# Kernel optimization log

Hardware: AMD Instinct MI355X
Metric: run time of the kernel (lower is better)

Reference implementation:

```python
import jax, jax.numpy as jnp
import numpy as np

B, S, D_IN, D_MODEL, H = 2, 2048, 1024, 1024, 16
DEPTH = D_MODEL // H


def setup_inputs() -> dict:
    key = jax.random.key(0)
    ks = jax.random.split(key, 12)
    f32 = jnp.float32
    scale = 0.02  # typical init scale for linear weights
    inp = {
        "v": jax.random.normal(ks[0], (B, S, D_IN), f32),
        "k": jax.random.normal(ks[1], (B, S, D_IN), f32),
        "q": jax.random.normal(ks[2], (B, S, D_IN), f32),
        # padding mask: 1 -> masked out, 0 -> keep; broadcastable to (B,H,Sq,Sk)
        "mask": jax.random.randint(ks[3], (B, 1, 1, S), 0, 2).astype(f32),
        # linear params stored as [in, out] so y = x @ W + b (matches torch Linear math)
        "Wq": jax.random.normal(ks[4], (D_IN, D_MODEL), f32) * scale,
        "bq": jnp.zeros((D_MODEL,), f32),
        "Wk": jax.random.normal(ks[5], (D_IN, D_MODEL), f32) * scale,
        "bk": jnp.zeros((D_MODEL,), f32),
        "Wv": jax.random.normal(ks[6], (D_IN, D_MODEL), f32) * scale,
        "bv": jnp.zeros((D_MODEL,), f32),
        "Wo": jax.random.normal(ks[7], (D_MODEL, D_MODEL), f32) * scale,
        "bo": jnp.zeros((D_MODEL,), f32),
    }
    return inp


def _split_heads(x):
    # [B, S, D_MODEL] -> [B, H, S, DEPTH]
    b = x.shape[0]
    return x.reshape(b, -1, H, DEPTH).transpose(0, 2, 1, 3)


def reference(v, k, q, mask, Wq, bq, Wk, bk, Wv, bv, Wo, bo):
    qh = _split_heads(q @ Wq + bq)   # [B,H,Sq,D]
    kh = _split_heads(k @ Wk + bk)   # [B,H,Sk,D]
    vh = _split_heads(v @ Wv + bv)   # [B,H,Sk,D]

    # scaled dot-product attention with additive mask (mask * -1e9)
    inv_sqrt_dk = 1.0 / jnp.sqrt(jnp.float32(DEPTH))
    logits = jnp.einsum('bhqd,bhkd->bhqk', qh, kh) * inv_sqrt_dk
    logits = logits + mask * (-1e9)
    attn = jax.nn.softmax(logits, axis=-1)          # [B,H,Sq,Sk]
    ctx = jnp.einsum('bhqk,bhkd->bhqd', attn, vh)   # [B,H,Sq,D]

    b = q.shape[0]
    concat = ctx.transpose(0, 2, 1, 3).reshape(b, -1, D_MODEL)  # [B,Sq,D_MODEL]
    out = concat @ Wo + bo
    return out, attn
```

## Files before the change

kernel.cpp:

```cpp
#include <hip/hip_runtime.h>
#include <cstdint>
#include <cstddef>

typedef __attribute__((ext_vector_type(4))) float f4;
typedef __attribute__((ext_vector_type(8))) short bf16x8;
typedef __attribute__((ext_vector_type(8))) unsigned short u16x8;
typedef unsigned long long u64;

__device__ __forceinline__ unsigned short f2bf(float x) {
    unsigned u = __float_as_uint(x);
    u += 0x7fffu + ((u >> 16) & 1u);
    return (unsigned short)(u >> 16);
}
__device__ __forceinline__ float bf2f(unsigned short h) {
    return __uint_as_float(((unsigned)h) << 16);
}
__device__ __forceinline__ float fast_exp2(float x) { return __builtin_amdgcn_exp2f(x); }
__device__ __forceinline__ float fast_log2(float x) { return __builtin_amdgcn_logf(x); }
__device__ __forceinline__ void gll16(const void* g, void* l) {
    __builtin_amdgcn_global_load_lds(
        (const __attribute__((address_space(1))) unsigned int*)g,
        (__attribute__((address_space(3))) unsigned int*)l, 16, 0, 0);
}
__device__ __forceinline__ f4 mfma16(bf16x8 a, bf16x8 b, f4 c) {
    return __builtin_amdgcn_mfma_f32_16x16x32_bf16(a, b, c, 0, 0, 0);
}

__global__ __launch_bounds__(256)
void prep_w_kernel(const float* __restrict__ Wq, const float* __restrict__ Wk,
                   const float* __restrict__ Wv, const float* __restrict__ Wo,
                   unsigned short* __restrict__ wt)
{
    const int w = blockIdx.z;
    const float* W = w == 0 ? Wq : (w == 1 ? Wk : (w == 2 ? Wv : Wo));
    unsigned short* hi = wt + (size_t)w * 1048576;

    const int kb = blockIdx.x << 6, nb = blockIdx.y << 6;
    __shared__ float T[64][68];
    const int tid = threadIdx.x;
    {
        const int r = tid >> 2, c0 = (tid & 3) << 4;
        const float* src = W + (size_t)(kb + r) * 1024 + nb + c0;
        *(f4*)&T[r][c0 + 0]  = *(const f4*)(src + 0);
        *(f4*)&T[r][c0 + 4]  = *(const f4*)(src + 4);
        *(f4*)&T[r][c0 + 8]  = *(const f4*)(src + 8);
        *(f4*)&T[r][c0 + 12] = *(const f4*)(src + 12);
    }
    __syncthreads();
    {
        const int n = tid & 63, ks = (tid >> 6) << 4;
        unsigned short vh[16];
        #pragma unroll
        for (int j = 0; j < 16; ++j) vh[j] = f2bf(T[ks + j][n]);
        const size_t dst = (size_t)(nb + n) * 1024 + kb + ks;
        *(u16x8*)(hi + dst)     = *(u16x8*)&vh[0];
        *(u16x8*)(hi + dst + 8) = *(u16x8*)&vh[8];
    }
}

__global__ __launch_bounds__(256)
void prep_a_kernel(const float* __restrict__ q, const float* __restrict__ k,
                   const float* __restrict__ v, unsigned short* __restrict__ a_hi)
{
    const int gid = blockIdx.x * 256 + threadIdx.x;
    const int z = gid >> 18;
    const int rem = gid & 262143;
    const float* src = z == 0 ? q : (z == 1 ? k : v);
    const size_t off = (size_t)rem << 4;
    const float* s = src + off;
    unsigned short* hi = a_hi + ((size_t)z << 22) + off;
    float xs[16];
    *(f4*)&xs[0]  = *(const f4*)(s + 0);
    *(f4*)&xs[4]  = *(const f4*)(s + 4);
    *(f4*)&xs[8]  = *(const f4*)(s + 8);
    *(f4*)&xs[12] = *(const f4*)(s + 12);
    unsigned short hv[16];
    #pragma unroll
    for (int j = 0; j < 16; ++j) hv[j] = f2bf(xs[j]);
    *(u16x8*)(hi + 0) = *(u16x8*)&hv[0];
    *(u16x8*)(hi + 8) = *(u16x8*)&hv[8];
}

__device__ __forceinline__ void gemm1_core(
    const unsigned short* __restrict__ AH, const unsigned short* __restrict__ WH,
    const float* __restrict__ bias, int bm, int bn, int mode,
    unsigned short* __restrict__ o_hi, float* __restrict__ o_f32, unsigned char* lds)
{
    unsigned char* As = lds;
    unsigned char* Bs = lds + 16384;

    const int tid = threadIdx.x, lane = tid & 63, wave = tid >> 6;
    const int wm = wave >> 1, wn = wave & 1;
    const int cx = lane & 15, lg = lane >> 4;
    const int l3 = lane >> 3, p3 = lane & 7;
    const int m0 = bm << 7, n0 = bn << 7;

    f4 acc[4][4];
    #pragma unroll
    for (int i = 0; i < 4; ++i)
        #pragma unroll
        for (int j = 0; j < 4; ++j) acc[i][j] = (f4){0.f, 0.f, 0.f, 0.f};

    #pragma unroll 1
    for (int k0 = 0; k0 < 1024; k0 += 64) {
        __syncthreads();
        #pragma unroll
        for (int c = 0; c < 4; ++c) {
            const int cb = (c << 2) + wave;
            const int row = (cb << 3) + l3;
            const int lgx = p3 ^ (row & 7);
            gll16(AH + (size_t)(m0 + row) * 1024 + k0 + (lgx << 3),
                  As + (cb << 10) + (lane << 4));
            gll16(WH + (size_t)(n0 + row) * 1024 + k0 + (lgx << 3),
                  Bs + (cb << 10) + (lane << 4));
        }
        __syncthreads();
        #pragma unroll
        for (int ks = 0; ks < 2; ++ks) {
            bf16x8 ah[4], bh[4];
            #pragma unroll
            for (int t = 0; t < 4; ++t) {
                const int r = (wm << 6) + (t << 4) + cx;
                ah[t] = *(const bf16x8*)(As + r * 128 + (((((ks << 2) + lg)) ^ (r & 7)) << 4));
                const int n = (wn << 6) + (t << 4) + cx;
                bh[t] = *(const bf16x8*)(Bs + n * 128 + (((((ks << 2) + lg)) ^ (n & 7)) << 4));
            }
            #pragma unroll
            for (int i = 0; i < 4; ++i)
                #pragma unroll
                for (int j = 0; j < 4; ++j)
                    acc[i][j] = mfma16(ah[i], bh[j], acc[i][j]);
        }
    }

    float bv4[4];
    #pragma unroll
    for (int j = 0; j < 4; ++j) bv4[j] = bias[n0 + (wn << 6) + (j << 4) + cx];

    #pragma unroll
    for (int i = 0; i < 4; ++i)
        #pragma unroll
        for (int j = 0; j < 4; ++j) {
            const int n = n0 + (wn << 6) + (j << 4) + cx;
            #pragma unroll
            for (int r = 0; r < 4; ++r) {
                const float val = acc[i][j][r] + bv4[j];
                const int m = m0 + (wm << 6) + (i << 4) + (lg << 2) + r;
                if (mode == 2) {
                    o_f32[(size_t)m * 1024 + n] = val;
                } else {
                    const int b = m >> 11, s = m & 2047, hh = n >> 6, d = n & 63;
                    o_hi[(((size_t)(b * 16 + hh)) * 2048 + s) * 64 + d] = f2bf(val);
                }
            }
        }
}

__global__ __launch_bounds__(256)
void qkv_gemm_kernel(const unsigned short* __restrict__ a_hi,
                     const unsigned short* __restrict__ wt,
                     const float* __restrict__ bq, const float* __restrict__ bk,
                     const float* __restrict__ bv,
                     unsigned short* __restrict__ q_hi, unsigned short* __restrict__ k_hi,
                     unsigned short* __restrict__ v_hi)
{
    __shared__ __align__(16) unsigned char lds[32768];
    const int f = blockIdx.x;
    const int id2 = (f & 7) * 96 + (f >> 3);
    const int z = id2 >> 8;
    const int rem = id2 & 255;
    const int bn = rem >> 5, bm = rem & 31;
    const unsigned short* AH = a_hi + ((size_t)z << 22);
    const unsigned short* WH = wt + (size_t)z * 1048576;
    const float* bias = z == 0 ? bq : (z == 1 ? bk : bv);
    unsigned short* ohi = z == 0 ? q_hi : (z == 1 ? k_hi : v_hi);
    gemm1_core(AH, WH, bias, bm, bn, 1, ohi, nullptr, lds);
}

__global__ __launch_bounds__(256)
void out_gemm_kernel(const unsigned short* __restrict__ ctx_hi,
                     const unsigned short* __restrict__ wt_o,
                     const float* __restrict__ bo, float* __restrict__ out)
{
    __shared__ __align__(16) unsigned char lds[32768];
    const int f = blockIdx.x;
    const int id2 = (f & 7) * 32 + (f >> 3);
    const int bn = id2 >> 5, bm = id2 & 31;
    gemm1_core(ctx_hi, wt_o, bo, bm, bn, 2, nullptr, out, lds);
}

__global__ __launch_bounds__(256, 3)
void attn_kernel(const unsigned short* __restrict__ q_hi, const unsigned short* __restrict__ k_hi,
                 const unsigned short* __restrict__ v_hi, const float* __restrict__ mask,
                 float* __restrict__ attn, unsigned short* __restrict__ ctx_hi)
{
    __shared__ __align__(16) unsigned char lds[49152];
    unsigned char* K1 = lds;
    unsigned char* Vs = lds + 16384;
    unsigned char* Ps = lds + 32768;
    float*         ML = (float*)(lds + 40960);

    const int f = blockIdx.x;
    const int swzf = (f & 7) * 128 + (f >> 3);
    const int bh = swzf >> 5;
    const int q0 = (swzf & 31) << 6;
    const int b = bh >> 4, h = bh & 15;
    const int tid = threadIdx.x, lane = tid & 63, wave = tid >> 6;
    const int cx = lane & 15, lg = lane >> 4;
    const int l3 = lane >> 3, p3 = lane & 7;
    const size_t base = (size_t)bh * 131072;
    const float* mg = mask + (size_t)b * 2048;

    constexpr float C2   = 0.18033688011112042f;
    constexpr float M2   = -1.4426950408889634e9f;
    constexpr float MFIX = 4.0f;

    {
        const int i0 = tid << 3;
        f4 mv0 = *(const f4*)(mg + i0);
        f4 mv1 = *(const f4*)(mg + i0 + 4);
        f4 w0, w1;
        #pragma unroll
        for (int j = 0; j < 4; ++j) { w0[j] = fmaf(mv0[j], M2, -MFIX); w1[j] = fmaf(mv1[j], M2, -MFIX); }
        *(f4*)(ML + i0) = w0;
        *(f4*)(ML + i0 + 4) = w1;
    }
    #pragma unroll
    for (int c = 0; c < 2; ++c) {
        const int cb = (c << 2) + wave;
        const int row = (cb << 3) + l3;
        const int lgx = p3 ^ (row & 7);
        gll16(q_hi + base + (size_t)(q0 + row) * 64 + (lgx << 3),
              Ps + (cb << 10) + (lane << 4));
        gll16(k_hi + base + (size_t)row * 64 + (lgx << 3),
              K1 + (cb << 10) + (lane << 4));
    }
    {
        u16x8 v0 = *(const u16x8*)(v_hi + base + (size_t)lane * 64 + (wave << 4));
        u16x8 v1 = *(const u16x8*)(v_hi + base + (size_t)lane * 64 + (wave << 4) + 8);
        const int slot = lane >> 3, sb = (lane & 7) << 1;
        #pragma unroll
        for (int j = 0; j < 8; ++j) {
            const int d = (wave << 4) + j;
            *(unsigned short*)(Vs + d * 128 + ((slot ^ (d & 7)) << 4) + sb) = (unsigned short)v0[j];
            const int d2 = d + 8;
            *(unsigned short*)(Vs + d2 * 128 + ((slot ^ (d2 & 7)) << 4) + sb) = (unsigned short)v1[j];
        }
    }
    __syncthreads();

    bf16x8 qb[2];
    {
        const int r = (wave << 4) + cx;
        const int mk = r & 7;
        #pragma unroll
        for (int ks = 0; ks < 2; ++ks)
            qb[ks] = *(const bf16x8*)(Ps + r * 128 + (((((ks << 2) + lg)) ^ mk) << 4));
    }

    float l_loc = 0.f;
    #pragma unroll 1
    for (int t = 0; t < 32; ++t) {
        const int p = t & 1;
        const int k0 = t << 6;
        if (t < 31) {
            #pragma unroll
            for (int c = 0; c < 2; ++c) {
                const int cb = (c << 2) + wave;
                const int row = (cb << 3) + l3;
                const int lgx = p3 ^ (row & 7);
                gll16(k_hi + base + (size_t)(k0 + 64 + row) * 64 + (lgx << 3),
                      K1 + ((p ^ 1) << 13) + (cb << 10) + (lane << 4));
            }
        }
        const unsigned char* Kc = K1 + (p << 13);
        #pragma unroll
        for (int nt = 0; nt < 4; ++nt) {
            const int kr = (nt << 4) + cx;
            const int mk = kr & 7;
            f4 s = (f4){0.f, 0.f, 0.f, 0.f};
            #pragma unroll
            for (int ks = 0; ks < 2; ++ks) {
                const bf16x8 kb = *(const bf16x8*)(Kc + kr * 128 + (((((ks << 2) + lg)) ^ mk) << 4));
                s = mfma16(kb, qb[ks], s);
            }
            const f4 mlv = *(const f4*)(ML + k0 + (nt << 4) + (lg << 2));
            l_loc += fast_exp2(fmaf(s[0], C2, mlv[0]))
                   + fast_exp2(fmaf(s[1], C2, mlv[1]))
                   + fast_exp2(fmaf(s[2], C2, mlv[2]))
                   + fast_exp2(fmaf(s[3], C2, mlv[3]));
        }
        asm volatile("s_waitcnt vmcnt(0) lgkmcnt(0)" ::: "memory");
        __builtin_amdgcn_s_barrier();
    }
    float ss = l_loc;
    ss += __shfl_xor(ss, 16);
    ss += __shfl_xor(ss, 32);
    const float ofs2 = fast_log2(ss);

    #pragma unroll
    for (int c = 0; c < 2; ++c) {
        const int cb = (c << 2) + wave;
        const int row = (cb << 3) + l3;
        const int lgx = p3 ^ (row & 7);
        gll16(k_hi + base + (size_t)row * 64 + (lgx << 3),
              K1 + (cb << 10) + (lane << 4));
    }
    {
        u16x8 v0 = *(const u16x8*)(v_hi + base + (size_t)lane * 64 + (wave << 4));
        u16x8 v1 = *(const u16x8*)(v_hi + base + (size_t)lane * 64 + (wave << 4) + 8);
        const int slot = lane >> 3, sb = (lane & 7) << 1;
        #pragma unroll
        for (int j = 0; j < 8; ++j) {
            const int d = (wave << 4) + j;
            *(unsigned short*)(Vs + d * 128 + ((slot ^ (d & 7)) << 4) + sb) = (unsigned short)v0[j];
            const int d2 = d + 8;
            *(unsigned short*)(Vs + d2 * 128 + ((slot ^ (d2 & 7)) << 4) + sb) = (unsigned short)v1[j];
        }
    }
    __syncthreads();

    f4 cacc[4];
    #pragma unroll
    for (int nt = 0; nt < 4; ++nt) cacc[nt] = (f4){0.f, 0.f, 0.f, 0.f};

    float* arow = attn + ((size_t)bh * 2048 + q0 + (wave << 4) + cx) * 2048;
    const unsigned psSwz = (unsigned)((cx & 7) << 4);

    #pragma unroll 1
    for (int t = 0; t < 32; ++t) {
        const int p = t & 1;
        const int k0 = t << 6;
        u16x8 vn0, vn1;
        if (t < 31) {
            #pragma unroll
            for (int c = 0; c < 2; ++c) {
                const int cb = (c << 2) + wave;
                const int row = (cb << 3) + l3;
                const int lgx = p3 ^ (row & 7);
                gll16(k_hi + base + (size_t)(k0 + 64 + row) * 64 + (lgx << 3),
                      K1 + ((p ^ 1) << 13) + (cb << 10) + (lane << 4));
            }
            vn0 = *(const u16x8*)(v_hi + base + (size_t)(k0 + 64 + lane) * 64 + (wave << 4));
            vn1 = *(const u16x8*)(v_hi + base + (size_t)(k0 + 64 + lane) * 64 + (wave << 4) + 8);
        }
        const unsigned char* Kc = K1 + (p << 13);
        f4 s[4];
        #pragma unroll
        for (int nt = 0; nt < 4; ++nt) {
            const int kr = (nt << 4) + cx;
            const int mk = kr & 7;
            s[nt] = (f4){0.f, 0.f, 0.f, 0.f};
            #pragma unroll
            for (int ks = 0; ks < 2; ++ks) {
                const bf16x8 kb = *(const bf16x8*)(Kc + kr * 128 + (((((ks << 2) + lg)) ^ mk) << 4));
                s[nt] = mfma16(kb, qb[ks], s[nt]);
            }
        }
        #pragma unroll
        for (int nt = 0; nt < 4; ++nt) {
            const f4 mlv = *(const f4*)(ML + k0 + (nt << 4) + (lg << 2));
            f4 pv;
            #pragma unroll
            for (int r = 0; r < 4; ++r)
                pv[r] = fast_exp2(fmaf(s[nt][r], C2, mlv[r]) - ofs2);
            *(f4*)(arow + k0 + (nt << 4) + (lg << 2)) = pv;
            const unsigned w0 = (unsigned)f2bf(pv[0]) | ((unsigned)f2bf(pv[1]) << 16);
            const unsigned w1 = (unsigned)f2bf(pv[2]) | ((unsigned)f2bf(pv[3]) << 16);
            const u64 packed = (u64)w0 | ((u64)w1 << 32);
            *(u64*)(Ps + (((wave << 4) + cx) * 128) +
                    ((unsigned)((nt << 5) + (lg << 3)) ^ psSwz)) = packed;
        }
        if (t < 31) {
            unsigned char* Vb = Vs + ((p ^ 1) << 13);
            const int slot = lane >> 3, sb = (lane & 7) << 1;
            #pragma unroll
            for (int j = 0; j < 8; ++j) {
                const int d = (wave << 4) + j;
                *(unsigned short*)(Vb + d * 128 + ((slot ^ (d & 7)) << 4) + sb) = (unsigned short)vn0[j];
                const int d2 = d + 8;
                *(unsigned short*)(Vb + d2 * 128 + ((slot ^ (d2 & 7)) << 4) + sb) = (unsigned short)vn1[j];
            }
        }
        #pragma unroll
        for (int ks = 0; ks < 2; ++ks) {
            const bf16x8 pa = *(const bf16x8*)(Ps + (((wave << 4) + cx) * 128) +
                                ((unsigned)((ks << 6) + (lg << 4)) ^ psSwz));
            #pragma unroll
            for (int nt = 0; nt < 4; ++nt) {
                const int dr = (nt << 4) + cx;
                const bf16x8 vb = *(const bf16x8*)(Vs + (p << 13) + dr * 128 +
                                    (((((ks << 2) + lg)) ^ (dr & 7)) << 4));
                cacc[nt] = mfma16(pa, vb, cacc[nt]);
            }
        }
        asm volatile("s_waitcnt vmcnt(4) lgkmcnt(0)" ::: "memory");
        __builtin_amdgcn_s_barrier();
    }

    #pragma unroll
    for (int nt = 0; nt < 4; ++nt)
        #pragma unroll
        for (int r = 0; r < 4; ++r) {
            const int srow = q0 + (wave << 4) + (lg << 2) + r;
            const int d = (h << 6) + (nt << 4) + cx;
            ctx_hi[((size_t)b * 2048 + srow) * 1024 + d] = f2bf(cacc[nt][r]);
        }
}

extern "C" void kernel_launch(void* const* d_in, const int* in_sizes, int n_in,
                              void* d_out, int out_size, void* d_ws, size_t ws_size,
                              hipStream_t stream)
{
    const float* v_in = (const float*)d_in[0];
    const float* k_in = (const float*)d_in[1];
    const float* q_in = (const float*)d_in[2];
    const float* mask = (const float*)d_in[3];
    const float* Wq = (const float*)d_in[4];
    const float* bq = (const float*)d_in[5];
    const float* Wk = (const float*)d_in[6];
    const float* bk = (const float*)d_in[7];
    const float* Wv = (const float*)d_in[8];
    const float* bv = (const float*)d_in[9];
    const float* Wo = (const float*)d_in[10];
    const float* bo = (const float*)d_in[11];

    float* out  = (float*)d_out;
    float* attn = out + (size_t)4194304;

    unsigned char* ws = (unsigned char*)d_ws;
    unsigned short* wt     = (unsigned short*)(ws);
    unsigned short* q_hi   = (unsigned short*)(ws + (size_t)(8)  * 1048576);
    unsigned short* k_hi   = (unsigned short*)(ws + (size_t)(16) * 1048576);
    unsigned short* v_hi   = (unsigned short*)(ws + (size_t)(24) * 1048576);
    unsigned short* ctx_hi = (unsigned short*)(ws + (size_t)(32) * 1048576);

    unsigned short* a_hi   = (unsigned short*)(attn + (size_t)60 * 1048576);

    prep_w_kernel<<<dim3(16, 16, 4), 256, 0, stream>>>(Wq, Wk, Wv, Wo, wt);
    prep_a_kernel<<<3072, 256, 0, stream>>>(q_in, k_in, v_in, a_hi);
    qkv_gemm_kernel<<<768, 256, 0, stream>>>(a_hi, wt, bq, bk, bv, q_hi, k_hi, v_hi);
    attn_kernel<<<1024, 256, 0, stream>>>(q_hi, k_hi, v_hi, mask, attn, ctx_hi);
    out_gemm_kernel<<<256, 256, 0, stream>>>(ctx_hi, wt + (size_t)3 * 1048576, bo, out);
}
```

Before: 299.0 us.

## Emit V transposed from QKV GEMM and async-load it; read mask from registers

The QKV GEMM now writes V in a per-head transposed [d][s] layout through a new store mode that packs four bf16 values per 8-byte store. The attention kernel can then stream V tiles into LDS with global_load_lds, the same path K uses, instead of register loads followed by scattered 2-byte LDS transposes. The mask LDS table is removed and mask values are prefetched into registers one tile ahead, cutting LDS to 40 KB so the launch bound can rise to 4 blocks per SM. Waitcnt thresholds are adjusted for the extra in-flight loads, and the mask transform is recomputed with an extra FMA per element.

```diff
diff --git a/kernel.cpp b/kernel.cpp
--- a/kernel.cpp
+++ b/kernel.cpp
@@ -142,16 +142,27 @@
         #pragma unroll
         for (int j = 0; j < 4; ++j) {
             const int n = n0 + (wn << 6) + (j << 4) + cx;
-            #pragma unroll
-            for (int r = 0; r < 4; ++r) {
-                const float val = acc[i][j][r] + bv4[j];
-                const int m = m0 + (wm << 6) + (i << 4) + (lg << 2) + r;
-                if (mode == 2) {
-                    o_f32[(size_t)m * 1024 + n] = val;
-                } else {
-                    const int b = m >> 11, s = m & 2047, hh = n >> 6, d = n & 63;
-                    o_hi[(((size_t)(b * 16 + hh)) * 2048 + s) * 64 + d] = f2bf(val);
+            const int mb = m0 + (wm << 6) + (i << 4) + (lg << 2);
+            if (mode == 2) {
+                #pragma unroll
+                for (int r = 0; r < 4; ++r)
+                    o_f32[(size_t)(mb + r) * 1024 + n] = acc[i][j][r] + bv4[j];
+            } else if (mode == 1) {
+                const int b = mb >> 11, hh = n >> 6, d = n & 63;
+                #pragma unroll
+                for (int r = 0; r < 4; ++r) {
+                    const int s = (mb + r) & 2047;
+                    o_hi[(((size_t)(b * 16 + hh)) * 2048 + s) * 64 + d] = f2bf(acc[i][j][r] + bv4[j]);
                 }
+            } else {
+                const int b = mb >> 11, s = mb & 2047;
+                const int hh = n >> 6, d = n & 63;
+                const unsigned short p0 = f2bf(acc[i][j][0] + bv4[j]);
+                const unsigned short p1 = f2bf(acc[i][j][1] + bv4[j]);
+                const unsigned short p2 = f2bf(acc[i][j][2] + bv4[j]);
+                const unsigned short p3v = f2bf(acc[i][j][3] + bv4[j]);
+                const u64 pk = (u64)p0 | ((u64)p1 << 16) | ((u64)p2 << 32) | ((u64)p3v << 48);
+                *(u64*)&o_hi[((((size_t)(b * 16 + hh)) * 64 + d) << 11) + s] = pk;
             }
         }
 }
@@ -162,7 +173,7 @@
                      const float* __restrict__ bq, const float* __restrict__ bk,
                      const float* __restrict__ bv,
                      unsigned short* __restrict__ q_hi, unsigned short* __restrict__ k_hi,
-                     unsigned short* __restrict__ v_hi)
+                     unsigned short* __restrict__ vT)
 {
     __shared__ __align__(16) unsigned char lds[32768];
     const int f = blockIdx.x;
@@ -173,8 +184,8 @@
     const unsigned short* AH = a_hi + ((size_t)z << 22);
     const unsigned short* WH = wt + (size_t)z * 1048576;
     const float* bias = z == 0 ? bq : (z == 1 ? bk : bv);
-    unsigned short* ohi = z == 0 ? q_hi : (z == 1 ? k_hi : v_hi);
-    gemm1_core(AH, WH, bias, bm, bn, 1, ohi, nullptr, lds);
+    unsigned short* ohi = z == 0 ? q_hi : (z == 1 ? k_hi : vT);
+    gemm1_core(AH, WH, bias, bm, bn, (z == 2) ? 3 : 1, ohi, nullptr, lds);
 }
 
 __global__ __launch_bounds__(256)
@@ -189,16 +200,15 @@
     gemm1_core(ctx_hi, wt_o, bo, bm, bn, 2, nullptr, out, lds);
 }
 
-__global__ __launch_bounds__(256, 3)
+__global__ __launch_bounds__(256, 4)
 void attn_kernel(const unsigned short* __restrict__ q_hi, const unsigned short* __restrict__ k_hi,
-                 const unsigned short* __restrict__ v_hi, const float* __restrict__ mask,
+                 const unsigned short* __restrict__ vT, const float* __restrict__ mask,
                  float* __restrict__ attn, unsigned short* __restrict__ ctx_hi)
 {
-    __shared__ __align__(16) unsigned char lds[49152];
+    __shared__ __align__(16) unsigned char lds[40960];
     unsigned char* K1 = lds;
     unsigned char* Vs = lds + 16384;
     unsigned char* Ps = lds + 32768;
-    float*         ML = (float*)(lds + 40960);
 
     const int f = blockIdx.x;
     const int swzf = (f & 7) * 128 + (f >> 3);
@@ -215,16 +225,6 @@
     constexpr float M2   = -1.4426950408889634e9f;
     constexpr float MFIX = 4.0f;
 
-    {
-        const int i0 = tid << 3;
-        f4 mv0 = *(const f4*)(mg + i0);
-        f4 mv1 = *(const f4*)(mg + i0 + 4);
-        f4 w0, w1;
-        #pragma unroll
-        for (int j = 0; j < 4; ++j) { w0[j] = fmaf(mv0[j], M2, -MFIX); w1[j] = fmaf(mv1[j], M2, -MFIX); }
-        *(f4*)(ML + i0) = w0;
-        *(f4*)(ML + i0 + 4) = w1;
-    }
     #pragma unroll
     for (int c = 0; c < 2; ++c) {
         const int cb = (c << 2) + wave;
@@ -235,19 +235,11 @@
         gll16(k_hi + base + (size_t)row * 64 + (lgx << 3),
               K1 + (cb << 10) + (lane << 4));
     }
-    {
-        u16x8 v0 = *(const u16x8*)(v_hi + base + (size_t)lane * 64 + (wave << 4));
-        u16x8 v1 = *(const u16x8*)(v_hi + base + (size_t)lane * 64 + (wave << 4) + 8);
-        const int slot = lane >> 3, sb = (lane & 7) << 1;
-        #pragma unroll
-        for (int j = 0; j < 8; ++j) {
-            const int d = (wave << 4) + j;
-            *(unsigned short*)(Vs + d * 128 + ((slot ^ (d & 7)) << 4) + sb) = (unsigned short)v0[j];
-            const int d2 = d + 8;
-            *(unsigned short*)(Vs + d2 * 128 + ((slot ^ (d2 & 7)) << 4) + sb) = (unsigned short)v1[j];
-        }
-    }
-    __syncthreads();
+    f4 mrc[4];
+    #pragma unroll
+    for (int nt = 0; nt < 4; ++nt) mrc[nt] = *(const f4*)(mg + (nt << 4) + (lg << 2));
+    asm volatile("s_waitcnt vmcnt(0)" ::: "memory");
+    __builtin_amdgcn_s_barrier();
 
     bf16x8 qb[2];
     {
@@ -263,6 +255,7 @@
     for (int t = 0; t < 32; ++t) {
         const int p = t & 1;
         const int k0 = t << 6;
+        f4 mrn[4];
         if (t < 31) {
             #pragma unroll
             for (int c = 0; c < 2; ++c) {
@@ -272,6 +265,9 @@
                 gll16(k_hi + base + (size_t)(k0 + 64 + row) * 64 + (lgx << 3),
                       K1 + ((p ^ 1) << 13) + (cb << 10) + (lane << 4));
             }
+            #pragma unroll
+            for (int nt = 0; nt < 4; ++nt)
+                mrn[nt] = *(const f4*)(mg + k0 + 64 + (nt << 4) + (lg << 2));
         }
         const unsigned char* Kc = K1 + (p << 13);
         #pragma unroll
@@ -284,19 +280,19 @@
                 const bf16x8 kb = *(const bf16x8*)(Kc + kr * 128 + (((((ks << 2) + lg)) ^ mk) << 4));
                 s = mfma16(kb, qb[ks], s);
             }
-            const f4 mlv = *(const f4*)(ML + k0 + (nt << 4) + (lg << 2));
-            l_loc += fast_exp2(fmaf(s[0], C2, mlv[0]))
-                   + fast_exp2(fmaf(s[1], C2, mlv[1]))
-                   + fast_exp2(fmaf(s[2], C2, mlv[2]))
-                   + fast_exp2(fmaf(s[3], C2, mlv[3]));
-        }
-        asm volatile("s_waitcnt vmcnt(0) lgkmcnt(0)" ::: "memory");
+            #pragma unroll
+            for (int r = 0; r < 4; ++r)
+                l_loc += fast_exp2(fmaf(s[r], C2, fmaf(mrc[nt][r], M2, -MFIX)));
+        }
+        #pragma unroll
+        for (int nt = 0; nt < 4; ++nt) mrc[nt] = mrn[nt];
+        asm volatile("s_waitcnt vmcnt(4)" ::: "memory");
         __builtin_amdgcn_s_barrier();
     }
-    float ss = l_loc;
-    ss += __shfl_xor(ss, 16);
-    ss += __shfl_xor(ss, 32);
-    const float ofs2 = fast_log2(ss);
+    float ssum = l_loc;
+    ssum += __shfl_xor(ssum, 16);
+    ssum += __shfl_xor(ssum, 32);
+    const float cofs = -MFIX - fast_log2(ssum);
 
     #pragma unroll
     for (int c = 0; c < 2; ++c) {
@@ -305,20 +301,13 @@
         const int lgx = p3 ^ (row & 7);
         gll16(k_hi + base + (size_t)row * 64 + (lgx << 3),
               K1 + (cb << 10) + (lane << 4));
-    }
-    {
-        u16x8 v0 = *(const u16x8*)(v_hi + base + (size_t)lane * 64 + (wave << 4));
-        u16x8 v1 = *(const u16x8*)(v_hi + base + (size_t)lane * 64 + (wave << 4) + 8);
-        const int slot = lane >> 3, sb = (lane & 7) << 1;
-        #pragma unroll
-        for (int j = 0; j < 8; ++j) {
-            const int d = (wave << 4) + j;
-            *(unsigned short*)(Vs + d * 128 + ((slot ^ (d & 7)) << 4) + sb) = (unsigned short)v0[j];
-            const int d2 = d + 8;
-            *(unsigned short*)(Vs + d2 * 128 + ((slot ^ (d2 & 7)) << 4) + sb) = (unsigned short)v1[j];
-        }
-    }
-    __syncthreads();
+        gll16(vT + base + ((size_t)row << 11) + (lgx << 3),
+              Vs + (cb << 10) + (lane << 4));
+    }
+    #pragma unroll
+    for (int nt = 0; nt < 4; ++nt) mrc[nt] = *(const f4*)(mg + (nt << 4) + (lg << 2));
+    asm volatile("s_waitcnt vmcnt(0)" ::: "memory");
+    __builtin_amdgcn_s_barrier();
 
     f4 cacc[4];
     #pragma unroll
@@ -331,7 +320,7 @@
     for (int t = 0; t < 32; ++t) {
         const int p = t & 1;
         const int k0 = t << 6;
-        u16x8 vn0, vn1;
+        f4 mrn[4];
         if (t < 31) {
             #pragma unroll
             for (int c = 0; c < 2; ++c) {
@@ -340,9 +329,12 @@
                 const int lgx = p3 ^ (row & 7);
                 gll16(k_hi + base + (size_t)(k0 + 64 + row) * 64 + (lgx << 3),
                       K1 + ((p ^ 1) << 13) + (cb << 10) + (lane << 4));
-            }
-            vn0 = *(const u16x8*)(v_hi + base + (size_t)(k0 + 64 + lane) * 64 + (wave << 4));
-            vn1 = *(const u16x8*)(v_hi + base + (size_t)(k0 + 64 + lane) * 64 + (wave << 4) + 8);
+                gll16(vT + base + ((size_t)row << 11) + k0 + 64 + (lgx << 3),
+                      Vs + ((p ^ 1) << 13) + (cb << 10) + (lane << 4));
+            }
+            #pragma unroll
+            for (int nt = 0; nt < 4; ++nt)
+                mrn[nt] = *(const f4*)(mg + k0 + 64 + (nt << 4) + (lg << 2));
         }
         const unsigned char* Kc = K1 + (p << 13);
         f4 s[4];
@@ -359,11 +351,10 @@
         }
         #pragma unroll
         for (int nt = 0; nt < 4; ++nt) {
-            const f4 mlv = *(const f4*)(ML + k0 + (nt << 4) + (lg << 2));
             f4 pv;
             #pragma unroll
             for (int r = 0; r < 4; ++r)
-                pv[r] = fast_exp2(fmaf(s[nt][r], C2, mlv[r]) - ofs2);
+                pv[r] = fast_exp2(fmaf(s[nt][r], C2, fmaf(mrc[nt][r], M2, cofs)));
             *(f4*)(arow + k0 + (nt << 4) + (lg << 2)) = pv;
             const unsigned w0 = (unsigned)f2bf(pv[0]) | ((unsigned)f2bf(pv[1]) << 16);
             const unsigned w1 = (unsigned)f2bf(pv[2]) | ((unsigned)f2bf(pv[3]) << 16);
@@ -371,17 +362,8 @@
             *(u64*)(Ps + (((wave << 4) + cx) * 128) +
                     ((unsigned)((nt << 5) + (lg << 3)) ^ psSwz)) = packed;
         }
-        if (t < 31) {
-            unsigned char* Vb = Vs + ((p ^ 1) << 13);
-            const int slot = lane >> 3, sb = (lane & 7) << 1;
-            #pragma unroll
-            for (int j = 0; j < 8; ++j) {
-                const int d = (wave << 4) + j;
-                *(unsigned short*)(Vb + d * 128 + ((slot ^ (d & 7)) << 4) + sb) = (unsigned short)vn0[j];
-                const int d2 = d + 8;
-                *(unsigned short*)(Vb + d2 * 128 + ((slot ^ (d2 & 7)) << 4) + sb) = (unsigned short)vn1[j];
-            }
-        }
+        #pragma unroll
+        for (int nt = 0; nt < 4; ++nt) mrc[nt] = mrn[nt];
         #pragma unroll
         for (int ks = 0; ks < 2; ++ks) {
             const bf16x8 pa = *(const bf16x8*)(Ps + (((wave << 4) + cx) * 128) +
@@ -394,7 +376,7 @@
                 cacc[nt] = mfma16(pa, vb, cacc[nt]);
             }
         }
-        asm volatile("s_waitcnt vmcnt(4) lgkmcnt(0)" ::: "memory");
+        asm volatile("s_waitcnt vmcnt(8)" ::: "memory");
         __builtin_amdgcn_s_barrier();
     }
 
@@ -432,14 +414,14 @@
     unsigned short* wt     = (unsigned short*)(ws);
     unsigned short* q_hi   = (unsigned short*)(ws + (size_t)(8)  * 1048576);
     unsigned short* k_hi   = (unsigned short*)(ws + (size_t)(16) * 1048576);
-    unsigned short* v_hi   = (unsigned short*)(ws + (size_t)(24) * 1048576);
+    unsigned short* vT     = (unsigned short*)(ws + (size_t)(24) * 1048576);
     unsigned short* ctx_hi = (unsigned short*)(ws + (size_t)(32) * 1048576);
 
     unsigned short* a_hi   = (unsigned short*)(attn + (size_t)60 * 1048576);
 
     prep_w_kernel<<<dim3(16, 16, 4), 256, 0, stream>>>(Wq, Wk, Wv, Wo, wt);
     prep_a_kernel<<<3072, 256, 0, stream>>>(q_in, k_in, v_in, a_hi);
-    qkv_gemm_kernel<<<768, 256, 0, stream>>>(a_hi, wt, bq, bk, bv, q_hi, k_hi, v_hi);
-    attn_kernel<<<1024, 256, 0, stream>>>(q_hi, k_hi, v_hi, mask, attn, ctx_hi);
+    qkv_gemm_kernel<<<768, 256, 0, stream>>>(a_hi, wt, bq, bk, bv, q_hi, k_hi, vT);
+    attn_kernel<<<1024, 256, 0, stream>>>(q_hi, k_hi, vT, mask, attn, ctx_hi);
     out_gemm_kernel<<<256, 256, 0, stream>>>(ctx_hi, wt + (size_t)3 * 1048576, bo, out);
 }
```

Result: slower. 308.3 us (+3.1%).
